# Kernel tuning notes

Measured on AMD Instinct MI355X. Metric: run time of the kernel, lower is better.

Reference implementation:

```python
import jax, jax.numpy as jnp
import numpy as np
from jax import lax

# Topology constants (windowed DAG: compute node i, at global index N_IN+i,
# reads the FANIN immediately preceding global node values).
N_IN = 16      # number of input nodes
FANIN = 16     # connections per compute node
N_NODES = 512  # topologically ordered compute nodes (hidden + output)
N_OUT = 64     # last N_OUT nodes in node_order are outputs
BATCH = 32768
T = N_IN + N_NODES  # total node count


def setup_inputs() -> dict:
    key = jax.random.key(0)
    k1, k2, k3, k4 = jax.random.split(key, 4)
    x = jax.random.normal(k1, (BATCH, N_IN), dtype=jnp.float32)
    # weights scaled down so tanh is not fully saturated through 512 layers
    weights = jax.random.normal(k2, (N_NODES, FANIN), dtype=jnp.float32) * 0.25
    biases = jax.random.normal(k3, (N_NODES,), dtype=jnp.float32) * 0.1
    responses = 1.0 + 0.1 * jax.random.normal(k4, (N_NODES,), dtype=jnp.float32)
    # src indices for node i: global indices [i, i+FANIN) (== previous FANIN nodes,
    # since N_IN == FANIN). Shape [N_NODES, FANIN], int32, all in [0, T).
    src_idx = (jnp.arange(N_NODES, dtype=jnp.int32)[:, None]
               + jnp.arange(FANIN, dtype=jnp.int32)[None, :]
               + (N_IN - FANIN))
    return {"x": x, "weights": weights, "biases": biases,
            "responses": responses, "src_idx": src_idx}


def _forward(x, weights, biases, responses, src_idx):
    B = x.shape[0]
    # values buffer [B, T]: inputs first, then compute nodes in topo order
    values0 = jnp.zeros((B, T), dtype=x.dtype).at[:, :N_IN].set(x)

    def body(values, xs):
        i, idx_row, w, b, r = xs
        src_vals = jnp.take(values, idx_row, axis=1)        # [B, FANIN] gather
        agg = src_vals @ w                                   # [B] weighted sum
        out = jnp.tanh(agg + b) * r                          # activation
        values = lax.dynamic_update_slice(values, out[:, None], (0, N_IN + i))
        return values, None

    ii = jnp.arange(N_NODES, dtype=jnp.int32)
    values, _ = lax.scan(body, values0, (ii, src_idx, weights, biases, responses))
    return values[:, T - N_OUT:]  # [B, N_OUT]


def reference(x, weights, biases, responses, src_idx):
    return _forward(x, weights, biases, responses, src_idx)
```

## Files before the change

### kernel.cpp

```cpp
#include <hip/hip_runtime.h>


typedef float v4f __attribute__((ext_vector_type(4)));

constexpr int kNodes  = 512;
constexpr int kNOut   = 64;
constexpr int kBatch  = 32768;
constexpr int kStrideF = 20;
constexpr int kLdsFloats = (kNodes + 3) * kStrideF + 4;
constexpr float kScale = 2.8853900817779268f;

#define PREF(S) {                                                             \
    asm volatile(                                                             \
      "ds_read_b128 %0, %5 offset:0\n\t"                                      \
      "ds_read_b128 %1, %5 offset:16\n\t"                                     \
      "ds_read_b128 %2, %5 offset:32\n\t"                                     \
      "ds_read_b128 %3, %5 offset:48\n\t"                                     \
      "ds_read_b128 %4, %5 offset:64"                                         \
      : "=&v"(q0[S]), "=&v"(q1[S]), "=&v"(q2[S]), "=&v"(q3[S]), "=&v"(q4[S])  \
      : "v"(a));                                                              \
    a += kStrideF * 4; }

#define WAITQ(S)                                                              \
    asm volatile("s_waitcnt lgkmcnt(15)"                                      \
      : "+v"(q0[S]), "+v"(q1[S]), "+v"(q2[S]), "+v"(q3[S]), "+v"(q4[S]));

#define NODE(K, A0,A1,A2,A3,A4,A5,A6,A7,A8,A9,A10,A11,A12,A13,A14,A15) {     \
    PREF(((K)+3)&3)                                                          \
    WAITQ((K)&3)                                                             \
    const int s = (K)&3;                                                     \
    v4f qa = q0[s], qb = q1[s], qc = q2[s], qd = q3[s], qm = q4[s];          \
    float p0 = fmaf(A0,  qa.x, qm.x);                                        \
    float p1 = A4  * qb.x;                                                   \
    float p2 = A8  * qc.x;                                                   \
    float p3 = A12 * qd.x;                                                   \
    p0 = fmaf(A1,  qa.y, p0);  p1 = fmaf(A5,  qb.y, p1);                     \
    p2 = fmaf(A9,  qc.y, p2);  p3 = fmaf(A13, qd.y, p3);                     \
    p0 = fmaf(A2,  qa.z, p0);  p1 = fmaf(A6,  qb.z, p1);                     \
    p2 = fmaf(A10, qc.z, p2);  p3 = fmaf(A14, qd.z, p3);                     \
    p0 = fmaf(A3,  qa.w, p0);  p1 = fmaf(A7,  qb.w, p1);                     \
    p2 = fmaf(A11, qc.w, p2);                                                \
    float pre = (p0 + p1) + (p2 + p3);                                       \
    float acc = fmaf(A15, qd.w, pre);          \
    float e = __builtin_amdgcn_exp2f(acc);                                   \
    float u = __builtin_amdgcn_rcpf(e + 1.0f);                               \
    A0 = fmaf(qm.z, u, qm.y); }

__global__ __launch_bounds__(128) void neat_fwd(
    const float* __restrict__ x,
    const float* __restrict__ w,
    const float* __restrict__ bias,
    const float* __restrict__ resp,
    float* __restrict__ out)
{
    __shared__ float lds[kLdsFloats];

    const int t = threadIdx.x;

    const float4* __restrict__ w4 = reinterpret_cast<const float4*>(w);
    #pragma unroll
    for (int j = 0; j < 16; ++j) {
        int i4 = t + j * 128;
        float4 v = w4[i4];
        int node = i4 >> 2, pos = (i4 & 3) << 2;
        float4 s = make_float4(v.x * kScale, v.y * kScale, v.z * kScale, v.w * kScale);
        *reinterpret_cast<float4*>(lds + node * kStrideF + pos) = s;
    }
    #pragma unroll
    for (int j = 0; j < 4; ++j) {
        int n = t + j * 128;
        float b = bias[n], r = resp[n];
        lds[n * kStrideF + 16] = b * kScale;
        lds[n * kStrideF + 17] = r;
        lds[n * kStrideF + 18] = -2.0f * r;
        lds[n * kStrideF + 19] = 0.0f;
    }

    const int b = blockIdx.x * blockDim.x + t;
    const float4* __restrict__ x4 = reinterpret_cast<const float4*>(x) + (size_t)b * 4;
    float4 a0 = x4[0], a1 = x4[1], a2 = x4[2], a3 = x4[3];
    float v0  = a0.x, v1  = a0.y, v2  = a0.z, v3  = a0.w;
    float v4  = a1.x, v5  = a1.y, v6  = a1.z, v7  = a1.w;
    float v8  = a2.x, v9  = a2.y, v10 = a2.z, v11 = a2.w;
    float v12 = a3.x, v13 = a3.y, v14 = a3.z, v15 = a3.w;

    float* __restrict__ op = out + (size_t)b * kNOut;

    __syncthreads();

    unsigned int a = (unsigned int)(unsigned long long)(&lds[0]);

    v4f q0[4], q1[4], q2[4], q3[4], q4[4];
    PREF(0) PREF(1) PREF(2)

    #pragma unroll 1
    for (int g = 0; g < 32; ++g) {
        NODE( 0, v0 ,v1 ,v2 ,v3 ,v4 ,v5 ,v6 ,v7 ,v8 ,v9 ,v10,v11,v12,v13,v14,v15)
        NODE( 1, v1 ,v2 ,v3 ,v4 ,v5 ,v6 ,v7 ,v8 ,v9 ,v10,v11,v12,v13,v14,v15,v0 )
        NODE( 2, v2 ,v3 ,v4 ,v5 ,v6 ,v7 ,v8 ,v9 ,v10,v11,v12,v13,v14,v15,v0 ,v1 )
        NODE( 3, v3 ,v4 ,v5 ,v6 ,v7 ,v8 ,v9 ,v10,v11,v12,v13,v14,v15,v0 ,v1 ,v2 )
        NODE( 4, v4 ,v5 ,v6 ,v7 ,v8 ,v9 ,v10,v11,v12,v13,v14,v15,v0 ,v1 ,v2 ,v3 )
        NODE( 5, v5 ,v6 ,v7 ,v8 ,v9 ,v10,v11,v12,v13,v14,v15,v0 ,v1 ,v2 ,v3 ,v4 )
        NODE( 6, v6 ,v7 ,v8 ,v9 ,v10,v11,v12,v13,v14,v15,v0 ,v1 ,v2 ,v3 ,v4 ,v5 )
        NODE( 7, v7 ,v8 ,v9 ,v10,v11,v12,v13,v14,v15,v0 ,v1 ,v2 ,v3 ,v4 ,v5 ,v6 )
        NODE( 8, v8 ,v9 ,v10,v11,v12,v13,v14,v15,v0 ,v1 ,v2 ,v3 ,v4 ,v5 ,v6 ,v7 )
        NODE( 9, v9 ,v10,v11,v12,v13,v14,v15,v0 ,v1 ,v2 ,v3 ,v4 ,v5 ,v6 ,v7 ,v8 )
        NODE(10, v10,v11,v12,v13,v14,v15,v0 ,v1 ,v2 ,v3 ,v4 ,v5 ,v6 ,v7 ,v8 ,v9 )
        NODE(11, v11,v12,v13,v14,v15,v0 ,v1 ,v2 ,v3 ,v4 ,v5 ,v6 ,v7 ,v8 ,v9 ,v10)
        NODE(12, v12,v13,v14,v15,v0 ,v1 ,v2 ,v3 ,v4 ,v5 ,v6 ,v7 ,v8 ,v9 ,v10,v11)
        NODE(13, v13,v14,v15,v0 ,v1 ,v2 ,v3 ,v4 ,v5 ,v6 ,v7 ,v8 ,v9 ,v10,v11,v12)
        NODE(14, v14,v15,v0 ,v1 ,v2 ,v3 ,v4 ,v5 ,v6 ,v7 ,v8 ,v9 ,v10,v11,v12,v13)
        NODE(15, v15,v0 ,v1 ,v2 ,v3 ,v4 ,v5 ,v6 ,v7 ,v8 ,v9 ,v10,v11,v12,v13,v14)
        if (g >= 28) {
            float4* o4 = reinterpret_cast<float4*>(op + (g - 28) * 16);
            o4[0] = make_float4(v0,  v1,  v2,  v3);
            o4[1] = make_float4(v4,  v5,  v6,  v7);
            o4[2] = make_float4(v8,  v9,  v10, v11);
            o4[3] = make_float4(v12, v13, v14, v15);
        }
    }

    asm volatile("s_waitcnt lgkmcnt(0)" ::: "memory");
}

extern "C" void kernel_launch(void* const* d_in, const int* in_sizes, int n_in,
                              void* d_out, int out_size, void* d_ws, size_t ws_size,
                              hipStream_t stream) {
    const float* x    = (const float*)d_in[0];
    const float* w    = (const float*)d_in[1];
    const float* bias = (const float*)d_in[2];
    const float* resp = (const float*)d_in[3];
    float* out = (float*)d_out;
    dim3 block(128);
    dim3 grid(kBatch / 128);
    hipLaunchKernelGGL(neat_fwd, grid, block, 0, stream, x, w, bias, resp, out);
}
```

Measured before the change: 98.67 us.

## Process two batch rows per thread with packed float2 FMAs

Each thread now handles two batch elements, one from each half of the batch, stored as two-wide float vectors. This lets the compiler emit packed FP32 FMA instructions, and each LDS weight read is shared by two rows. Block size drops to 64 threads while the grid size stays the same, which halves the total thread count and the LDS reads per element. The cost is higher register pressure and fewer waves to hide latency along the serial 512-node dependency chain.

```diff
diff --git a/kernel.cpp b/kernel.cpp
--- a/kernel.cpp
+++ b/kernel.cpp
@@ -2,13 +2,17 @@
 
 
 typedef float v4f __attribute__((ext_vector_type(4)));
+typedef float v2f __attribute__((ext_vector_type(2)));
 
 constexpr int kNodes  = 512;
 constexpr int kNOut   = 64;
 constexpr int kBatch  = 32768;
+constexpr int kHalf   = kBatch / 2;
 constexpr int kStrideF = 20;
 constexpr int kLdsFloats = (kNodes + 3) * kStrideF + 4;
 constexpr float kScale = 2.8853900817779268f;
+
+__device__ __forceinline__ v2f sp(float f) { v2f r; r.x = f; r.y = f; return r; }
 
 #define PREF(S) {                                                             \
     asm volatile(                                                             \
@@ -30,23 +34,31 @@
     WAITQ((K)&3)                                                             \
     const int s = (K)&3;                                                     \
     v4f qa = q0[s], qb = q1[s], qc = q2[s], qd = q3[s], qm = q4[s];          \
-    float p0 = fmaf(A0,  qa.x, qm.x);                                        \
-    float p1 = A4  * qb.x;                                                   \
-    float p2 = A8  * qc.x;                                                   \
-    float p3 = A12 * qd.x;                                                   \
-    p0 = fmaf(A1,  qa.y, p0);  p1 = fmaf(A5,  qb.y, p1);                     \
-    p2 = fmaf(A9,  qc.y, p2);  p3 = fmaf(A13, qd.y, p3);                     \
-    p0 = fmaf(A2,  qa.z, p0);  p1 = fmaf(A6,  qb.z, p1);                     \
-    p2 = fmaf(A10, qc.z, p2);  p3 = fmaf(A14, qd.z, p3);                     \
-    p0 = fmaf(A3,  qa.w, p0);  p1 = fmaf(A7,  qb.w, p1);                     \
-    p2 = fmaf(A11, qc.w, p2);                                                \
-    float pre = (p0 + p1) + (p2 + p3);                                       \
-    float acc = fmaf(A15, qd.w, pre);          \
-    float e = __builtin_amdgcn_exp2f(acc);                                   \
-    float u = __builtin_amdgcn_rcpf(e + 1.0f);                               \
-    A0 = fmaf(qm.z, u, qm.y); }
+    v2f p0 = __builtin_elementwise_fma(A0,  sp(qa.x), sp(qm.x));             \
+    v2f p1 = A4  * sp(qb.x);                                                 \
+    v2f p2 = A8  * sp(qc.x);                                                 \
+    v2f p3 = A12 * sp(qd.x);                                                 \
+    p0 = __builtin_elementwise_fma(A1,  sp(qa.y), p0);                       \
+    p1 = __builtin_elementwise_fma(A5,  sp(qb.y), p1);                       \
+    p2 = __builtin_elementwise_fma(A9,  sp(qc.y), p2);                       \
+    p3 = __builtin_elementwise_fma(A13, sp(qd.y), p3);                       \
+    p0 = __builtin_elementwise_fma(A2,  sp(qa.z), p0);                       \
+    p1 = __builtin_elementwise_fma(A6,  sp(qb.z), p1);                       \
+    p2 = __builtin_elementwise_fma(A10, sp(qc.z), p2);                       \
+    p3 = __builtin_elementwise_fma(A14, sp(qd.z), p3);                       \
+    p0 = __builtin_elementwise_fma(A3,  sp(qa.w), p0);                       \
+    p1 = __builtin_elementwise_fma(A7,  sp(qb.w), p1);                       \
+    p2 = __builtin_elementwise_fma(A11, sp(qc.w), p2);                       \
+    v2f pre = (p0 + p1) + (p2 + p3);                                         \
+    v2f acc = __builtin_elementwise_fma(A15, sp(qd.w), pre);                 \
+    float eA = __builtin_amdgcn_exp2f(acc.x);                                \
+    float eB = __builtin_amdgcn_exp2f(acc.y);                                \
+    float uA = __builtin_amdgcn_rcpf(eA + 1.0f);                             \
+    float uB = __builtin_amdgcn_rcpf(eB + 1.0f);                             \
+    A0.x = fmaf(qm.z, uA, qm.y);                                             \
+    A0.y = fmaf(qm.z, uB, qm.y); }
 
-__global__ __launch_bounds__(128) void neat_fwd(
+__global__ __launch_bounds__(64) void neat_fwd(
     const float* __restrict__ x,
     const float* __restrict__ w,
     const float* __restrict__ bias,
@@ -59,16 +71,16 @@
 
     const float4* __restrict__ w4 = reinterpret_cast<const float4*>(w);
     #pragma unroll
-    for (int j = 0; j < 16; ++j) {
-        int i4 = t + j * 128;
+    for (int j = 0; j < 32; ++j) {
+        int i4 = t + j * 64;
         float4 v = w4[i4];
         int node = i4 >> 2, pos = (i4 & 3) << 2;
         float4 s = make_float4(v.x * kScale, v.y * kScale, v.z * kScale, v.w * kScale);
         *reinterpret_cast<float4*>(lds + node * kStrideF + pos) = s;
     }
     #pragma unroll
-    for (int j = 0; j < 4; ++j) {
-        int n = t + j * 128;
+    for (int j = 0; j < 8; ++j) {
+        int n = t + j * 64;
         float b = bias[n], r = resp[n];
         lds[n * kStrideF + 16] = b * kScale;
         lds[n * kStrideF + 17] = r;
@@ -76,15 +88,19 @@
         lds[n * kStrideF + 19] = 0.0f;
     }
 
-    const int b = blockIdx.x * blockDim.x + t;
-    const float4* __restrict__ x4 = reinterpret_cast<const float4*>(x) + (size_t)b * 4;
-    float4 a0 = x4[0], a1 = x4[1], a2 = x4[2], a3 = x4[3];
-    float v0  = a0.x, v1  = a0.y, v2  = a0.z, v3  = a0.w;
-    float v4  = a1.x, v5  = a1.y, v6  = a1.z, v7  = a1.w;
-    float v8  = a2.x, v9  = a2.y, v10 = a2.z, v11 = a2.w;
-    float v12 = a3.x, v13 = a3.y, v14 = a3.z, v15 = a3.w;
+    const int e0 = blockIdx.x * 64 + t;
+    const float4* __restrict__ xa = reinterpret_cast<const float4*>(x) + (size_t)e0 * 4;
+    const float4* __restrict__ xb = xa + (size_t)kHalf * 4;
+    float4 a0 = xa[0], a1 = xa[1], a2 = xa[2], a3 = xa[3];
+    float4 b0 = xb[0], b1 = xb[1], b2 = xb[2], b3 = xb[3];
+    v2f v0, v1, v2, v3, v4, v5, v6, v7, v8, v9, v10, v11, v12, v13, v14, v15;
+    v0.x=a0.x; v1.x=a0.y; v2.x=a0.z; v3.x=a0.w; v4.x=a1.x; v5.x=a1.y; v6.x=a1.z; v7.x=a1.w;
+    v8.x=a2.x; v9.x=a2.y; v10.x=a2.z; v11.x=a2.w; v12.x=a3.x; v13.x=a3.y; v14.x=a3.z; v15.x=a3.w;
+    v0.y=b0.x; v1.y=b0.y; v2.y=b0.z; v3.y=b0.w; v4.y=b1.x; v5.y=b1.y; v6.y=b1.z; v7.y=b1.w;
+    v8.y=b2.x; v9.y=b2.y; v10.y=b2.z; v11.y=b2.w; v12.y=b3.x; v13.y=b3.y; v14.y=b3.z; v15.y=b3.w;
 
-    float* __restrict__ op = out + (size_t)b * kNOut;
+    float* __restrict__ opA = out + (size_t)e0 * kNOut;
+    float* __restrict__ opB = opA + (size_t)kHalf * kNOut;
 
     __syncthreads();
 
@@ -112,11 +128,16 @@
         NODE(14, v14,v15,v0 ,v1 ,v2 ,v3 ,v4 ,v5 ,v6 ,v7 ,v8 ,v9 ,v10,v11,v12,v13)
         NODE(15, v15,v0 ,v1 ,v2 ,v3 ,v4 ,v5 ,v6 ,v7 ,v8 ,v9 ,v10,v11,v12,v13,v14)
         if (g >= 28) {
-            float4* o4 = reinterpret_cast<float4*>(op + (g - 28) * 16);
-            o4[0] = make_float4(v0,  v1,  v2,  v3);
-            o4[1] = make_float4(v4,  v5,  v6,  v7);
-            o4[2] = make_float4(v8,  v9,  v10, v11);
-            o4[3] = make_float4(v12, v13, v14, v15);
+            float4* oa = reinterpret_cast<float4*>(opA + (g - 28) * 16);
+            oa[0] = make_float4(v0.x,  v1.x,  v2.x,  v3.x);
+            oa[1] = make_float4(v4.x,  v5.x,  v6.x,  v7.x);
+            oa[2] = make_float4(v8.x,  v9.x,  v10.x, v11.x);
+            oa[3] = make_float4(v12.x, v13.x, v14.x, v15.x);
+            float4* ob = reinterpret_cast<float4*>(opB + (g - 28) * 16);
+            ob[0] = make_float4(v0.y,  v1.y,  v2.y,  v3.y);
+            ob[1] = make_float4(v4.y,  v5.y,  v6.y,  v7.y);
+            ob[2] = make_float4(v8.y,  v9.y,  v10.y, v11.y);
+            ob[3] = make_float4(v12.y, v13.y, v14.y, v15.y);
         }
     }
 
@@ -131,7 +152,7 @@
     const float* bias = (const float*)d_in[2];
     const float* resp = (const float*)d_in[3];
     float* out = (float*)d_out;
-    dim3 block(128);
+    dim3 block(64);
     dim3 grid(kBatch / 128);
     hipLaunchKernelGGL(neat_fwd, grid, block, 0, stream, x, w, bias, resp, out);
 }
```

Result: slower. 108.7 us (+10.1%).
